# Performance work log

Hardware: AMD Instinct MI355X
Metric: run time of the kernel (lower is better)

The kernel has to match this reference:

```python
import jax, jax.numpy as jnp
import numpy as np

N, E, G = 50000, 1600000, 512
IN_DIM, HEADS, C1, C2, HIDDEN = 128, 3, 32, 32, 512
NEG_SLOPE = 0.2
EPS = 1e-16


def _glorot(key, shape):
    fan_in = shape[0]
    return jax.random.normal(key, shape, dtype=jnp.float32) / np.sqrt(fan_in)


def setup_inputs() -> dict:
    key = jax.random.key(0)
    ks = jax.random.split(key, 16)
    x = jax.random.normal(ks[0], (N, IN_DIM), dtype=jnp.float32)
    edge_index = jax.random.randint(ks[1], (2, E), 0, N, dtype=jnp.int64)
    batch = (jnp.arange(N, dtype=jnp.int64) * G) // N  # sorted, all graphs non-empty
    d1, d2 = HEADS * C1, HEADS * C2
    return {
        "x": x,
        "W_l1": _glorot(ks[2], (IN_DIM, d1)), "b_l1": jnp.zeros((d1,), jnp.float32),
        "W_r1": _glorot(ks[3], (IN_DIM, d1)), "b_r1": jnp.zeros((d1,), jnp.float32),
        "att1": _glorot(ks[4], (HEADS, C1)), "bias1": jnp.zeros((d1,), jnp.float32),
        "W_l2": _glorot(ks[5], (d1, d2)), "b_l2": jnp.zeros((d2,), jnp.float32),
        "W_r2": _glorot(ks[6], (d1, d2)), "b_r2": jnp.zeros((d2,), jnp.float32),
        "att2": _glorot(ks[7], (HEADS, C2)), "bias2": jnp.zeros((d2,), jnp.float32),
        "W_fc1": _glorot(ks[8], (d1 + d2, HIDDEN)), "b_fc1": jnp.zeros((HIDDEN,), jnp.float32),
        "W_fc2": _glorot(ks[9], (HIDDEN, 2)), "b_fc2": jnp.zeros((2,), jnp.float32),
        "edge_index": edge_index,
        "batch": batch,
    }


def gatv2_conv(xin, src, dst, W_l, b_l, W_r, b_r, att, bias, heads, out_c):
    n = xin.shape[0]
    x_l = (xin @ W_l + b_l).reshape(n, heads, out_c)  # source-side projection
    x_r = (xin @ W_r + b_r).reshape(n, heads, out_c)  # target-side projection
    e = jax.nn.leaky_relu(x_l[src] + x_r[dst], NEG_SLOPE)  # [E', H, C]
    logits = jnp.einsum("ehc,hc->eh", e, att)  # [E', H]
    m = jax.ops.segment_max(logits, dst, num_segments=n)
    a = jnp.exp(logits - m[dst])
    denom = jax.ops.segment_sum(a, dst, num_segments=n)
    alpha = a / (denom[dst] + EPS)  # per-destination edge softmax (PyG semantics)
    out = jax.ops.segment_sum(x_l[src] * alpha[:, :, None], dst, num_segments=n)
    return out.reshape(n, heads * out_c) + bias


def reference(x, W_l1, b_l1, W_r1, b_r1, att1, bias1,
              W_l2, b_l2, W_r2, b_r2, att2, bias2,
              W_fc1, b_fc1, W_fc2, b_fc2, edge_index, batch):
    n = x.shape[0]
    loop = jnp.arange(n, dtype=edge_index.dtype)
    src = jnp.concatenate([edge_index[0], loop])  # PyG GATv2Conv adds self-loops
    dst = jnp.concatenate([edge_index[1], loop])
    h1 = jnp.tanh(gatv2_conv(x, src, dst, W_l1, b_l1, W_r1, b_r1, att1, bias1, HEADS, C1))
    h2 = jnp.tanh(gatv2_conv(h1, src, dst, W_l2, b_l2, W_r2, b_r2, att2, bias2, HEADS, C2))
    h = jnp.concatenate([h1, h2], axis=1)  # [N, (C1+C2)*H]
    first_idx = jnp.searchsorted(batch, jnp.arange(G, dtype=batch.dtype))  # first node of each graph
    pooled = h[first_idx]  # [G, (C1+C2)*H]
    hidden = jax.nn.relu(pooled @ W_fc1 + b_fc1)
    logits = hidden @ W_fc2 + b_fc2
    return jax.nn.log_softmax(logits, axis=1)
```

## Files before the change

### kernel.cpp

```cpp
#include <hip/hip_runtime.h>
#include <hip/hip_bf16.h>
#include <hip/hip_fp16.h>
#include <math.h>

#define NN 50000
#define EE 1600000
#define GG 512
#define INDIM 128
#define HEADS 3
#define CC 32
#define DD 96
#define HID 512
#define NEG 0.2f
#define NEGM1 (NEG - 1.0f)
#define EPS_DEN 1e-16f
#define CAP 128
#define MNEG -1e30f
#define NBW 1568

#define OFF_WL1   0
#define OFF_BL1   12288
#define OFF_WR1   12384
#define OFF_BR1   24672
#define OFF_ATT1  24768
#define OFF_BIAS1 24864
#define OFF_WL2   24960
#define OFF_BL2   34176
#define OFF_WR2   34272
#define OFF_BR2   43488
#define OFF_ATT2  43584
#define OFF_BIAS2 43680
#define OFF_WFC1  43776
#define OFF_BFC1  142080
#define OFF_WFC2  142592
#define OFF_BFC2  143616
#define P_TOTAL   143744

typedef _Float16 h8 __attribute__((ext_vector_type(8)));
typedef float f4 __attribute__((ext_vector_type(4)));

static __device__ __forceinline__ float bf2f(__hip_bfloat16 v) { return __bfloat162float(v); }

static __device__ __forceinline__ int getI(const void* p, long long i, bool w64) {
    return w64 ? ((const int*)p)[2 * i] : ((const int*)p)[i];
}

static __device__ __forceinline__ void load4(const void* p, int base, int e0, bool w64, int* v) {
    const int4* q = (const int4*)p;
    if (w64) {
        int4 a = q[(base + e0) >> 1];
        int4 b = q[((base + e0) >> 1) + 1];
        v[0] = a.x; v[1] = a.z; v[2] = b.x; v[3] = b.z;
    } else {
        int4 a = q[(base + e0) >> 2];
        v[0] = a.x; v[1] = a.y; v[2] = a.z; v[3] = a.w;
    }
}

static __device__ __forceinline__ bool testbit(const unsigned* b, int i) {
    return (b[i >> 5] >> (i & 31)) & 1u;
}

__global__ void detect_kernel(const void* __restrict__ x, const void* __restrict__ ei,
                              int* __restrict__ flags)
{
    __shared__ int wild, zcnt;
    if (threadIdx.x == 0) { wild = 0; zcnt = 0; }
    __syncthreads();
    int w = 0, z = 0;
    const __hip_bfloat16* xb = (const __hip_bfloat16*)x;
    for (int i = threadIdx.x; i < 4096; i += 256) {
        float v = bf2f(xb[i]);
        if (!(fabsf(v) <= 1e6f)) w++;
    }
    const int* e32 = (const int*)ei;
    for (int i = threadIdx.x; i < 4096; i += 256) {
        if (e32[2 * i + 1] == 0) z++;
    }
    atomicAdd(&wild, w);
    atomicAdd(&zcnt, z);
    __syncthreads();
    if (threadIdx.x == 0) {
        flags[0] = (wild < 64) ? 1 : 0;
        flags[1] = (zcnt > 4000) ? 1 : 0;
    }
}

struct ParamTab { const void* p[16]; int sz[16]; int off[16]; };

__global__ void convert_params_kernel(ParamTab t, const int* __restrict__ flags,
                                      float* __restrict__ P)
{
    const int which = blockIdx.y;
    const int n = t.sz[which];
    const void* src = t.p[which];
    float* dst = P + t.off[which];
    const bool isbf = flags[0] != 0;
    for (int i = blockIdx.x * 256 + threadIdx.x; i < n; i += gridDim.x * 256) {
        dst[i] = isbf ? bf2f(((const __hip_bfloat16*)src)[i]) : ((const float*)src)[i];
    }
}

__global__ void build_bswz_kernel(const float* __restrict__ P, int offWl, int offWr, int KC,
                                  __half* __restrict__ B)
{
    int idx = blockIdx.x * 256 + threadIdx.x;
    int total = 12 * KC * 64;
    if (idx >= total) return;
    int lane = idx & 63;
    int t = idx >> 6;
    int kc = t % KC;
    int ntile = t / KC;
    int n = ntile * 16 + (lane & 15);
    int kbase = kc * 32 + (lane >> 4) * 8;
    const float* Wsrc = (n < 96) ? (P + offWl) : (P + offWr);
    int n2 = (n < 96) ? n : n - 96;
    __half* dst = B + (size_t)idx * 8;
#pragma unroll
    for (int j = 0; j < 8; j++) dst[j] = __float2half(Wsrc[(kbase + j) * 96 + n2]);
}

__global__ void build_bswz_fc_kernel(const float* __restrict__ P, __half* __restrict__ B)
{
    int idx = blockIdx.x * 256 + threadIdx.x;
    const int total = 32 * 6 * 64;
    if (idx >= total) return;
    int lane = idx & 63;
    int t = idx >> 6;
    int kc = t % 6;
    int ntile = t / 6;
    int n = ntile * 16 + (lane & 15);
    int kbase = kc * 32 + (lane >> 4) * 8;
    const float* W = P + OFF_WFC1;
    __half* dst = B + (size_t)idx * 8;
#pragma unroll
    for (int j = 0; j < 8; j++) dst[j] = __float2half(W[(kbase + j) * HID + n]);
}

__global__ void firstpool_kernel(const void* __restrict__ batch, const int* __restrict__ flags,
                                 int* __restrict__ first, unsigned* __restrict__ pb,
                                 unsigned* __restrict__ nb)
{
    int i = blockIdx.x * 256 + threadIdx.x;
    if (i >= NN) return;
    const bool w64 = flags[1] != 0;
    int b = getI(batch, i, w64);
    if (i == 0 || getI(batch, i - 1, w64) != b) {
        first[b] = i;
        atomicOr(&pb[i >> 5], 1u << (i & 31));
        atomicOr(&nb[i >> 5], 1u << (i & 31));
    }
}

__global__ void mark_needed_kernel(const void* __restrict__ ei, const int* __restrict__ flags,
                                   const unsigned* __restrict__ pb, unsigned* __restrict__ nb)
{
    int e0 = (blockIdx.x * 256 + threadIdx.x) * 4;
    if (e0 >= EE) return;
    const bool w64 = flags[1] != 0;
    int s4[4], d4[4];
    load4(ei, EE, e0, w64, d4);
    load4(ei, 0, e0, w64, s4);
#pragma unroll
    for (int j = 0; j < 4; j++)
        if (testbit(pb, d4[j])) atomicOr(&nb[s4[j] >> 5], 1u << (s4[j] & 31));
}

__global__ void compact_kernel(const unsigned* __restrict__ nb, int* __restrict__ list,
                               int* __restrict__ cnt)
{
    int i = blockIdx.x * 256 + threadIdx.x;
    if (i >= NN) return;
    if (testbit(nb, i)) list[atomicAdd(cnt, 1)] = i;
}

__global__ void scatter_fixed_kernel(const void* __restrict__ ei, const int* __restrict__ flags,
                                     const unsigned* __restrict__ nb,
                                     int* __restrict__ deg, int* __restrict__ csr)
{
    int e0 = (blockIdx.x * 256 + threadIdx.x) * 4;
    if (e0 >= EE) return;
    const bool w64 = flags[1] != 0;
    int s4[4], d4[4];
    load4(ei, EE, e0, w64, d4);
    load4(ei, 0, e0, w64, s4);
#pragma unroll
    for (int j = 0; j < 4; j++) {
        int dst = d4[j];
        if (!testbit(nb, dst)) continue;
        int pos = atomicAdd(&deg[dst], 1);
        if (pos < CAP) csr[(size_t)dst * CAP + pos] = s4[j];
    }
}

template <int KDIM, int MODE>
__global__ __launch_bounds__(256) void proj_mfma_kernel(
    const void* __restrict__ Ain, const __half* __restrict__ Bswz,
    const int* __restrict__ list, const int* __restrict__ cnt,
    const float* __restrict__ P, const int* __restrict__ flags, int offBl, int offBr,
    __half* __restrict__ xl, float* __restrict__ xr)
{
    constexpr int KC = KDIM / 32;
    __shared__ __half Bs[12 * KC * 64 * 8];
    const int tid = threadIdx.x;
    const int limit = MODE ? *cnt : NN;
    const int blockBase = blockIdx.x * 64;
    if (blockBase >= limit) return;

    {
        const int chunks = 12 * KC * 64;
        for (int i = tid; i < chunks; i += 256)
            reinterpret_cast<f4*>(Bs)[i] = reinterpret_cast<const f4*>(Bswz)[i];
    }
    __syncthreads();

    const int wave = tid >> 6;
    const int lane = tid & 63;
    const int base = blockBase + wave * 16;
    if (base >= limit) return;

    const int q = lane >> 4;
    const int mlane = lane & 15;

    int aIdx = base + mlane;
    int aRow;
    if (MODE) aRow = (aIdx < limit) ? list[aIdx] : list[limit - 1];
    else      aRow = (aIdx < limit) ? aIdx : 0;

    h8 a[KC];
    if (MODE == 1) {
        const h8* arow = reinterpret_cast<const h8*>((const __half*)Ain + (size_t)aRow * KDIM);
#pragma unroll
        for (int kc = 0; kc < KC; kc++) a[kc] = arow[kc * 4 + q];
    } else if (flags[0]) {
        const int4* arow = reinterpret_cast<const int4*>((const ushort*)Ain + (size_t)aRow * KDIM);
#pragma unroll
        for (int kc = 0; kc < KC; kc++) {
            int4 r = arow[kc * 4 + q];
            int ws[4] = {r.x, r.y, r.z, r.w};
#pragma unroll
            for (int i = 0; i < 4; i++) {
                a[kc][2 * i]     = (_Float16)__int_as_float(ws[i] << 16);
                a[kc][2 * i + 1] = (_Float16)__int_as_float(ws[i] & 0xffff0000);
            }
        }
    } else {
        const f4* arow = reinterpret_cast<const f4*>((const float*)Ain + (size_t)aRow * KDIM);
#pragma unroll
        for (int kc = 0; kc < KC; kc++) {
            f4 r0 = arow[kc * 8 + q * 2];
            f4 r1 = arow[kc * 8 + q * 2 + 1];
#pragma unroll
            for (int i = 0; i < 4; i++) {
                a[kc][i]     = (_Float16)r0[i];
                a[kc][4 + i] = (_Float16)r1[i];
            }
        }
    }

    int sRow[4];
#pragma unroll
    for (int r = 0; r < 4; r++) {
        int si = base + q * 4 + r;
        sRow[r] = (si < limit) ? (MODE ? list[si] : si) : -1;
    }

    const h8* Bf = reinterpret_cast<const h8*>(Bs);
#pragma unroll
    for (int ntile = 0; ntile < 12; ntile++) {
        int n = ntile * 16 + mlane;
        float bv = (n < 96) ? P[offBl + n] : P[offBr + n - 96];
        f4 acc = {bv, bv, bv, bv};
#pragma unroll
        for (int kc = 0; kc < KC; kc++) {
            h8 b = Bf[(ntile * KC + kc) * 64 + lane];
            acc = __builtin_amdgcn_mfma_f32_16x16x32_f16(a[kc], b, acc, 0, 0, 0);
        }
#pragma unroll
        for (int r = 0; r < 4; r++) {
            if (sRow[r] < 0) continue;
            if (n < 96) xl[(size_t)sRow[r] * DD + n] = __float2half(acc[r]);
            else        xr[(size_t)sRow[r] * DD + (n - 96)] = acc[r];
        }
    }
}

template <int OUTMODE>
__global__ __launch_bounds__(256) void fused_edge_kernel(
    const int* __restrict__ csr, const int* __restrict__ deg,
    const int* __restrict__ list, const int* __restrict__ cnt,
    const __half* __restrict__ xl, const float* __restrict__ xr,
    const float* __restrict__ P, int offAtt, int offBias,
    __half* __restrict__ out)
{
    const int lane = threadIdx.x & 63;
    const int c = lane & 31;
    const int eo = lane >> 5;
    const int w0 = (blockIdx.x * 256 + threadIdx.x) >> 6;
    const int nw = (gridDim.x * 256) >> 6;
    const int limit = (OUTMODE == 0) ? *cnt : GG;
    const int items = limit * 3;

    for (int item = w0; item < items; item += nw) {
        const int li = item / 3;
        const int h = item - li * 3;
        const int n = list[li];
        const int hc = h * CC + c;
        const __half* xlb = xl + hc;

        const float attc = P[offAtt + hc];
        const float xr_c = xr[(size_t)n * DD + hc];

        float m, d, o;
        {
            float xls = __half2float(xlb[n * DD]);
            float s = xls + xr_c;
            s = fmaf(fminf(s, 0.0f), NEGM1, s);
            float p = s * attc;
#pragma unroll
            for (int off = 16; off; off >>= 1) p += __shfl_xor(p, off, 32);
            if (eo == 0) { m = p; d = 1.0f; o = xls; }
            else         { m = MNEG; d = 0.0f; o = 0.0f; }
        }

        const int* row = csr + (size_t)n * CAP;
        const int end = min(deg[n], CAP);
        int k = eo;
        for (; k + 6 < end; k += 8) {
            int s0 = row[k], s1 = row[k + 2], s2 = row[k + 4], s3 = row[k + 6];
            float x0 = __half2float(xlb[s0 * DD]);
            float x1 = __half2float(xlb[s1 * DD]);
            float x2 = __half2float(xlb[s2 * DD]);
            float x3 = __half2float(xlb[s3 * DD]);
            float t0 = x0 + xr_c; t0 = fmaf(fminf(t0, 0.0f), NEGM1, t0);
            float t1 = x1 + xr_c; t1 = fmaf(fminf(t1, 0.0f), NEGM1, t1);
            float t2 = x2 + xr_c; t2 = fmaf(fminf(t2, 0.0f), NEGM1, t2);
            float t3 = x3 + xr_c; t3 = fmaf(fminf(t3, 0.0f), NEGM1, t3);
            float q0 = t0 * attc, q1 = t1 * attc, q2 = t2 * attc, q3 = t3 * attc;
#pragma unroll
            for (int off = 16; off; off >>= 1) {
                q0 += __shfl_xor(q0, off, 32);
                q1 += __shfl_xor(q1, off, 32);
                q2 += __shfl_xor(q2, off, 32);
                q3 += __shfl_xor(q3, off, 32);
            }
            if (q0 <= m) { float e = __expf(q0 - m); d += e; o += e * x0; }
            else         { float r2 = __expf(m - q0); d = d * r2 + 1.0f; o = o * r2 + x0; m = q0; }
            if (q1 <= m) { float e = __expf(q1 - m); d += e; o += e * x1; }
            else         { float r2 = __expf(m - q1); d = d * r2 + 1.0f; o = o * r2 + x1; m = q1; }
            if (q2 <= m) { float e = __expf(q2 - m); d += e; o += e * x2; }
            else         { float r2 = __expf(m - q2); d = d * r2 + 1.0f; o = o * r2 + x2; m = q2; }
            if (q3 <= m) { float e = __expf(q3 - m); d += e; o += e * x3; }
            else         { float r2 = __expf(m - q3); d = d * r2 + 1.0f; o = o * r2 + x3; m = q3; }
        }
        for (; k < end; k += 2) {
            int src = row[k];
            float xv = __half2float(xlb[src * DD]);
            float s = xv + xr_c;
            s = fmaf(fminf(s, 0.0f), NEGM1, s);
            float p = s * attc;
#pragma unroll
            for (int off = 16; off; off >>= 1) p += __shfl_xor(p, off, 32);
            if (p <= m) { float e = __expf(p - m); d += e; o += e * xv; }
            else        { float r2 = __expf(m - p); d = d * r2 + 1.0f; o = o * r2 + xv; m = p; }
        }

        float m2 = __shfl_xor(m, 32);
        float d2 = __shfl_xor(d, 32);
        float o2 = __shfl_xor(o, 32);
        float nm = fmaxf(m, m2);
        float e1 = __expf(m - nm), e2 = __expf(m2 - nm);
        d = d * e1 + d2 * e2;
        o = o * e1 + o2 * e2;

        float res = tanhf(o / (d + EPS_DEN) + P[offBias + hc]);
        if (eo == 0) {
            if (OUTMODE == 0) out[(size_t)n * DD + hc] = __float2half(res);
            else              out[(size_t)li * 192 + 96 + hc] = __float2half(res);
        }
    }
}

__global__ void gatherA_kernel(const __half* __restrict__ h1h, const int* __restrict__ first,
                               __half* __restrict__ A)
{
    int idx = blockIdx.x * 256 + threadIdx.x;
    if (idx >= GG * DD) return;
    int g = idx / DD, c = idx - g * DD;
    A[(size_t)g * 192 + c] = h1h[(size_t)first[g] * DD + c];
}

__global__ __launch_bounds__(256) void mlp_mfma_kernel(
    const __half* __restrict__ A, const __half* __restrict__ Bfc,
    const float* __restrict__ P, const int* __restrict__ flags, void* __restrict__ outv)
{
    const int tid = threadIdx.x;
    const int wave = tid >> 6, lane = tid & 63;
    const int q = lane >> 4, ml = lane & 15;
    const int rowbase = blockIdx.x * 64 + wave * 16;

    h8 a[6];
    const h8* arow = reinterpret_cast<const h8*>(A + (size_t)(rowbase + ml) * 192);
#pragma unroll
    for (int kc = 0; kc < 6; kc++) a[kc] = arow[kc * 4 + q];

    const h8* Bf = reinterpret_cast<const h8*>(Bfc);
    const float* w2 = P + OFF_WFC2;
    float p0[4] = {0, 0, 0, 0}, p1[4] = {0, 0, 0, 0};
    for (int nt = 0; nt < 32; nt++) {
        int n = nt * 16 + ml;
        float bv = P[OFF_BFC1 + n];
        f4 acc = {bv, bv, bv, bv};
#pragma unroll
        for (int kc = 0; kc < 6; kc++)
            acc = __builtin_amdgcn_mfma_f32_16x16x32_f16(a[kc], Bf[(nt * 6 + kc) * 64 + lane], acc, 0, 0, 0);
        float w20 = w2[2 * n], w21 = w2[2 * n + 1];
#pragma unroll
        for (int r = 0; r < 4; r++) {
            float hdn = fmaxf(acc[r], 0.0f);
            p0[r] = fmaf(hdn, w20, p0[r]);
            p1[r] = fmaf(hdn, w21, p1[r]);
        }
    }
#pragma unroll
    for (int off = 1; off <= 8; off <<= 1) {
#pragma unroll
        for (int r = 0; r < 4; r++) {
            p0[r] += __shfl_xor(p0[r], off);
            p1[r] += __shfl_xor(p1[r], off);
        }
    }
    if (ml == 0) {
        float b0 = P[OFF_BFC2], b1 = P[OFF_BFC2 + 1];
#pragma unroll
        for (int r = 0; r < 4; r++) {
            int g = rowbase + q * 4 + r;
            float l0 = p0[r] + b0, l1 = p1[r] + b1;
            float mx = fmaxf(l0, l1);
            float lse = mx + logf(__expf(l0 - mx) + __expf(l1 - mx));
            if (flags[0]) {
                ((__hip_bfloat16*)outv)[g * 2 + 0] = __float2bfloat16(l0 - lse);
                ((__hip_bfloat16*)outv)[g * 2 + 1] = __float2bfloat16(l1 - lse);
            } else {
                ((float*)outv)[g * 2 + 0] = l0 - lse;
                ((float*)outv)[g * 2 + 1] = l1 - lse;
            }
        }
    }
}

extern "C" void kernel_launch(void* const* d_in, const int* in_sizes, int n_in,
                              void* d_out, int out_size, void* d_ws, size_t ws_size,
                              hipStream_t stream)
{
    const void* x     = d_in[0];
    const void* ei    = d_in[17];
    const void* batch = d_in[18];

    float* ws   = (float*)d_ws;
    float* P    = ws;
    float* xr   = P + P_TOTAL;

    __half* hp   = (__half*)(xr + (size_t)NN * DD);
    __half* xlh  = hp;
    __half* xl2h = xlh + (size_t)NN * DD;
    __half* h1h  = xl2h + (size_t)NN * DD;
    __half* A    = h1h + (size_t)NN * DD;
    __half* B1   = A + (size_t)GG * 192;
    __half* B2   = B1 + 24576;
    __half* Bfc  = B2 + 18432;

    int* ip       = (int*)(Bfc + 98304);
    int* deg      = ip;
    unsigned* pb  = (unsigned*)(deg + NN);
    unsigned* nb  = pb + NBW;
    int* cnt      = (int*)(nb + NBW);
    int* csr      = cnt + 4;
    int* list     = csr + (size_t)NN * CAP;
    int* first    = list + NN;
    int* flags    = first + GG;

    ParamTab t;
    const int sz[16]  = {12288, 96, 12288, 96, 96, 96, 9216, 96, 9216, 96, 96, 96, 98304, 512, 1024, 2};
    const int off[16] = {OFF_WL1, OFF_BL1, OFF_WR1, OFF_BR1, OFF_ATT1, OFF_BIAS1,
                         OFF_WL2, OFF_BL2, OFF_WR2, OFF_BR2, OFF_ATT2, OFF_BIAS2,
                         OFF_WFC1, OFF_BFC1, OFF_WFC2, OFF_BFC2};
    for (int i = 0; i < 16; i++) { t.p[i] = d_in[1 + i]; t.sz[i] = sz[i]; t.off[i] = off[i]; }

    const int edge4B = (EE / 4 + 255) / 256;
    const int nodeB = (NN + 255) / 256;
    const int mprojB = (NN + 63) / 64;
    const int fuse1B = 2048;
    const int fuse2B = (GG * 3) / 4;

    detect_kernel<<<1, 256, 0, stream>>>(x, ei, flags);
    convert_params_kernel<<<dim3(96, 16), 256, 0, stream>>>(t, flags, P);
    build_bswz_kernel<<<12, 256, 0, stream>>>(P, OFF_WL1, OFF_WR1, 4, B1);
    build_bswz_kernel<<<9, 256, 0, stream>>>(P, OFF_WL2, OFF_WR2, 3, B2);
    build_bswz_fc_kernel<<<48, 256, 0, stream>>>(P, Bfc);
    (void)hipMemsetAsync(deg, 0, (size_t)(NN + 2 * NBW + 4) * sizeof(int), stream);

    firstpool_kernel<<<nodeB, 256, 0, stream>>>(batch, flags, first, pb, nb);
    mark_needed_kernel<<<edge4B, 256, 0, stream>>>(ei, flags, pb, nb);
    compact_kernel<<<nodeB, 256, 0, stream>>>(nb, list, cnt);

    scatter_fixed_kernel<<<edge4B, 256, 0, stream>>>(ei, flags, nb, deg, csr);

    proj_mfma_kernel<INDIM, 0><<<mprojB, 256, 0, stream>>>(x, B1, nullptr, nullptr,
                                                           P, flags, OFF_BL1, OFF_BR1, xlh, xr);
    fused_edge_kernel<0><<<fuse1B, 256, 0, stream>>>(csr, deg, list, cnt, xlh, xr,
                                                     P, OFF_ATT1, OFF_BIAS1, h1h);

    proj_mfma_kernel<DD, 1><<<mprojB, 256, 0, stream>>>(h1h, B2, list, cnt,
                                                        P, flags, OFF_BL2, OFF_BR2, xl2h, xr);
    fused_edge_kernel<1><<<fuse2B, 256, 0, stream>>>(csr, deg, first, nullptr, xl2h, xr,
                                                     P, OFF_ATT2, OFF_BIAS2, A);

    gatherA_kernel<<<(GG * DD + 255) / 256, 256, 0, stream>>>(h1h, first, A);
    mlp_mfma_kernel<<<GG / 64, 256, 0, stream>>>(A, Bfc, P, flags, d_out);
}
```

Before: 297.5 us.

## Merge setup and preprocessing kernels to cut launch count

Several small setup kernels (parameter conversion, three B-swizzle builds, memset, first-node pooling) are collapsed into one multi-task setup kernel that reads raw inputs directly, so the full weights are no longer staged as fp32. The needed-node bitmask, built with atomicOr, becomes an int array written with plain stores. The compaction step now runs as an extra grid dimension of the scatter kernel. The gatherA kernel is removed: the MLP kernel reads the h1 rows via first[] and the layer-2 output from a smaller A2 buffer. The aim is to cut launch overhead and serialization, at the cost of a larger needed array and branchy multi-task kernels.

```diff
diff --git a/kernel.cpp b/kernel.cpp
--- a/kernel.cpp
+++ b/kernel.cpp
@@ -18,23 +18,18 @@
 #define MNEG -1e30f
 #define NBW 1568
 
-#define OFF_WL1   0
-#define OFF_BL1   12288
-#define OFF_WR1   12384
-#define OFF_BR1   24672
-#define OFF_ATT1  24768
-#define OFF_BIAS1 24864
-#define OFF_WL2   24960
-#define OFF_BL2   34176
-#define OFF_WR2   34272
-#define OFF_BR2   43488
-#define OFF_ATT2  43584
-#define OFF_BIAS2 43680
-#define OFF_WFC1  43776
-#define OFF_BFC1  142080
-#define OFF_WFC2  142592
-#define OFF_BFC2  143616
-#define P_TOTAL   143744
+#define PS_BL1   0
+#define PS_BR1   96
+#define PS_ATT1  192
+#define PS_BIAS1 288
+#define PS_BL2   384
+#define PS_BR2   480
+#define PS_ATT2  576
+#define PS_BIAS2 672
+#define PS_BFC1  768
+#define PS_WFC2  1280
+#define PS_BFC2  2304
+#define PS_TOTAL 2308
 
 typedef _Float16 h8 __attribute__((ext_vector_type(8)));
 typedef float f4 __attribute__((ext_vector_type(4)));
@@ -43,6 +38,10 @@
 
 static __device__ __forceinline__ int getI(const void* p, long long i, bool w64) {
     return w64 ? ((const int*)p)[2 * i] : ((const int*)p)[i];
+}
+
+static __device__ __forceinline__ float rawf(const void* p, int i, bool isbf) {
+    return isbf ? bf2f(((const __hip_bfloat16*)p)[i]) : ((const float*)p)[i];
 }
 
 static __device__ __forceinline__ void load4(const void* p, int base, int e0, bool w64, int* v) {
@@ -86,74 +85,88 @@
     }
 }
 
-struct ParamTab { const void* p[16]; int sz[16]; int off[16]; };
-
-__global__ void convert_params_kernel(ParamTab t, const int* __restrict__ flags,
-                                      float* __restrict__ P)
-{
-    const int which = blockIdx.y;
-    const int n = t.sz[which];
-    const void* src = t.p[which];
-    float* dst = P + t.off[which];
+struct SetupArgs {
+    const void *wl1, *wr1, *wl2, *wr2, *wfc1;
+    const void *bl1, *br1, *att1, *bias1, *bl2, *br2, *att2, *bias2, *bfc1, *wfc2, *bfc2;
+    const void *batch;
+};
+
+__global__ void setup_kernel(SetupArgs a, const int* __restrict__ flags,
+                             float* __restrict__ P, __half* __restrict__ B1,
+                             __half* __restrict__ B2, __half* __restrict__ Bfc,
+                             int* __restrict__ deg, int* __restrict__ needed,
+                             int* __restrict__ first, unsigned* __restrict__ pb,
+                             int* __restrict__ cnt)
+{
+    const int task = blockIdx.y;
+    const int idx = blockIdx.x * 256 + threadIdx.x;
     const bool isbf = flags[0] != 0;
-    for (int i = blockIdx.x * 256 + threadIdx.x; i < n; i += gridDim.x * 256) {
-        dst[i] = isbf ? bf2f(((const __hip_bfloat16*)src)[i]) : ((const float*)src)[i];
-    }
-}
-
-__global__ void build_bswz_kernel(const float* __restrict__ P, int offWl, int offWr, int KC,
-                                  __half* __restrict__ B)
-{
-    int idx = blockIdx.x * 256 + threadIdx.x;
-    int total = 12 * KC * 64;
-    if (idx >= total) return;
-    int lane = idx & 63;
-    int t = idx >> 6;
-    int kc = t % KC;
-    int ntile = t / KC;
-    int n = ntile * 16 + (lane & 15);
-    int kbase = kc * 32 + (lane >> 4) * 8;
-    const float* Wsrc = (n < 96) ? (P + offWl) : (P + offWr);
-    int n2 = (n < 96) ? n : n - 96;
-    __half* dst = B + (size_t)idx * 8;
-#pragma unroll
-    for (int j = 0; j < 8; j++) dst[j] = __float2half(Wsrc[(kbase + j) * 96 + n2]);
-}
-
-__global__ void build_bswz_fc_kernel(const float* __restrict__ P, __half* __restrict__ B)
-{
-    int idx = blockIdx.x * 256 + threadIdx.x;
-    const int total = 32 * 6 * 64;
-    if (idx >= total) return;
-    int lane = idx & 63;
-    int t = idx >> 6;
-    int kc = t % 6;
-    int ntile = t / 6;
-    int n = ntile * 16 + (lane & 15);
-    int kbase = kc * 32 + (lane >> 4) * 8;
-    const float* W = P + OFF_WFC1;
-    __half* dst = B + (size_t)idx * 8;
-#pragma unroll
-    for (int j = 0; j < 8; j++) dst[j] = __float2half(W[(kbase + j) * HID + n]);
-}
-
-__global__ void firstpool_kernel(const void* __restrict__ batch, const int* __restrict__ flags,
-                                 int* __restrict__ first, unsigned* __restrict__ pb,
-                                 unsigned* __restrict__ nb)
-{
-    int i = blockIdx.x * 256 + threadIdx.x;
-    if (i >= NN) return;
-    const bool w64 = flags[1] != 0;
-    int b = getI(batch, i, w64);
-    if (i == 0 || getI(batch, i - 1, w64) != b) {
-        first[b] = i;
-        atomicOr(&pb[i >> 5], 1u << (i & 31));
-        atomicOr(&nb[i >> 5], 1u << (i & 31));
+
+    if (task == 0) {
+        if (idx == 0) *cnt = 0;
+        if (idx >= PS_TOTAL) return;
+        const void* src; int rel;
+        if (idx < 768) {
+            int k = idx / 96; rel = idx - k * 96;
+            const void* s8[8] = {a.bl1, a.br1, a.att1, a.bias1, a.bl2, a.br2, a.att2, a.bias2};
+            src = s8[k];
+        } else if (idx < 1280) { src = a.bfc1; rel = idx - 768; }
+        else if (idx < 2304)   { src = a.wfc2; rel = idx - 1280; }
+        else if (idx < 2306)   { src = a.bfc2; rel = idx - 2304; }
+        else return;
+        P[idx] = rawf(src, rel, isbf);
+    } else if (task == 1 || task == 2) {
+        const int KC = (task == 1) ? 4 : 3;
+        const int total = 12 * KC * 64;
+        if (idx >= total) return;
+        int lane = idx & 63, t = idx >> 6;
+        int kc = t % KC, ntile = t / KC;
+        int n = ntile * 16 + (lane & 15);
+        int kbase = kc * 32 + (lane >> 4) * 8;
+        const void* W = (task == 1) ? (n < 96 ? a.wl1 : a.wr1) : (n < 96 ? a.wl2 : a.wr2);
+        int n2 = (n < 96) ? n : n - 96;
+        __half* dst = ((task == 1) ? B1 : B2) + (size_t)idx * 8;
+#pragma unroll
+        for (int j = 0; j < 8; j++) dst[j] = __float2half(rawf(W, (kbase + j) * 96 + n2, isbf));
+    } else if (task == 3) {
+        const int total = 32 * 6 * 64;
+        if (idx >= total) return;
+        int lane = idx & 63, t = idx >> 6;
+        int kc = t % 6, ntile = t / 6;
+        int n = ntile * 16 + (lane & 15);
+        int kbase = kc * 32 + (lane >> 4) * 8;
+        __half* dst = Bfc + (size_t)idx * 8;
+#pragma unroll
+        for (int j = 0; j < 8; j++) dst[j] = __float2half(rawf(a.wfc1, (kbase + j) * HID + n, isbf));
+    } else if (task == 4) {
+        int i0 = idx * 4;
+#pragma unroll
+        for (int j = 0; j < 4; j++) if (i0 + j < NN) deg[i0 + j] = 0;
+    } else if (task == 5) {
+        if (idx >= NN) return;
+        const bool w64 = flags[1] != 0;
+        int b = getI(a.batch, idx, w64);
+        bool isf = (idx == 0) || (getI(a.batch, idx - 1, w64) != b);
+        needed[idx] = isf ? 1 : 0;
+        if (isf) first[b] = idx;
+    } else {
+        if (idx >= NBW) return;
+        const bool w64 = flags[1] != 0;
+        unsigned word = 0;
+        int prev = (idx == 0) ? -1 : getI(a.batch, idx * 32 - 1, w64);
+        for (int bit = 0; bit < 32; bit++) {
+            int i = idx * 32 + bit;
+            if (i >= NN) break;
+            int b = getI(a.batch, i, w64);
+            if (i == 0 || b != prev) word |= (1u << bit);
+            prev = b;
+        }
+        pb[idx] = word;
     }
 }
 
 __global__ void mark_needed_kernel(const void* __restrict__ ei, const int* __restrict__ flags,
-                                   const unsigned* __restrict__ pb, unsigned* __restrict__ nb)
+                                   const unsigned* __restrict__ pb, int* __restrict__ needed)
 {
     int e0 = (blockIdx.x * 256 + threadIdx.x) * 4;
     if (e0 >= EE) return;
@@ -163,21 +176,20 @@
     load4(ei, 0, e0, w64, s4);
 #pragma unroll
     for (int j = 0; j < 4; j++)
-        if (testbit(pb, d4[j])) atomicOr(&nb[s4[j] >> 5], 1u << (s4[j] & 31));
-}
-
-__global__ void compact_kernel(const unsigned* __restrict__ nb, int* __restrict__ list,
-                               int* __restrict__ cnt)
-{
-    int i = blockIdx.x * 256 + threadIdx.x;
-    if (i >= NN) return;
-    if (testbit(nb, i)) list[atomicAdd(cnt, 1)] = i;
-}
-
-__global__ void scatter_fixed_kernel(const void* __restrict__ ei, const int* __restrict__ flags,
-                                     const unsigned* __restrict__ nb,
-                                     int* __restrict__ deg, int* __restrict__ csr)
-{
+        if (testbit(pb, d4[j])) needed[s4[j]] = 1;
+}
+
+__global__ void scatter_compact_kernel(const void* __restrict__ ei, const int* __restrict__ flags,
+                                       const int* __restrict__ needed,
+                                       int* __restrict__ deg, int* __restrict__ csr,
+                                       int* __restrict__ list, int* __restrict__ cnt)
+{
+    if (blockIdx.y == 1) {
+        int i = blockIdx.x * 256 + threadIdx.x;
+        if (i >= NN) return;
+        if (needed[i]) list[atomicAdd(cnt, 1)] = i;
+        return;
+    }
     int e0 = (blockIdx.x * 256 + threadIdx.x) * 4;
     if (e0 >= EE) return;
     const bool w64 = flags[1] != 0;
@@ -187,7 +199,7 @@
 #pragma unroll
     for (int j = 0; j < 4; j++) {
         int dst = d4[j];
-        if (!testbit(nb, dst)) continue;
+        if (!needed[dst]) continue;
         int pos = atomicAdd(&deg[dst], 1);
         if (pos < CAP) csr[(size_t)dst * CAP + pos] = s4[j];
     }
@@ -376,40 +388,38 @@
         float res = tanhf(o / (d + EPS_DEN) + P[offBias + hc]);
         if (eo == 0) {
             if (OUTMODE == 0) out[(size_t)n * DD + hc] = __float2half(res);
-            else              out[(size_t)li * 192 + 96 + hc] = __float2half(res);
-        }
-    }
-}
-
-__global__ void gatherA_kernel(const __half* __restrict__ h1h, const int* __restrict__ first,
-                               __half* __restrict__ A)
-{
-    int idx = blockIdx.x * 256 + threadIdx.x;
-    if (idx >= GG * DD) return;
-    int g = idx / DD, c = idx - g * DD;
-    A[(size_t)g * 192 + c] = h1h[(size_t)first[g] * DD + c];
+            else              out[(size_t)li * DD + hc] = __float2half(res);
+        }
+    }
 }
 
 __global__ __launch_bounds__(256) void mlp_mfma_kernel(
-    const __half* __restrict__ A, const __half* __restrict__ Bfc,
+    const __half* __restrict__ h1h, const __half* __restrict__ A2,
+    const int* __restrict__ first, const __half* __restrict__ Bfc,
     const float* __restrict__ P, const int* __restrict__ flags, void* __restrict__ outv)
 {
     const int tid = threadIdx.x;
     const int wave = tid >> 6, lane = tid & 63;
     const int q = lane >> 4, ml = lane & 15;
     const int rowbase = blockIdx.x * 64 + wave * 16;
+    const int g16 = rowbase + ml;
 
     h8 a[6];
-    const h8* arow = reinterpret_cast<const h8*>(A + (size_t)(rowbase + ml) * 192);
-#pragma unroll
-    for (int kc = 0; kc < 6; kc++) a[kc] = arow[kc * 4 + q];
+    {
+        const h8* l = reinterpret_cast<const h8*>(h1h + (size_t)first[g16] * DD);
+#pragma unroll
+        for (int kc = 0; kc < 3; kc++) a[kc] = l[kc * 4 + q];
+        const h8* r = reinterpret_cast<const h8*>(A2 + (size_t)g16 * DD);
+#pragma unroll
+        for (int kc = 3; kc < 6; kc++) a[kc] = r[(kc - 3) * 4 + q];
+    }
 
     const h8* Bf = reinterpret_cast<const h8*>(Bfc);
-    const float* w2 = P + OFF_WFC2;
+    const float* w2 = P + PS_WFC2;
     float p0[4] = {0, 0, 0, 0}, p1[4] = {0, 0, 0, 0};
     for (int nt = 0; nt < 32; nt++) {
         int n = nt * 16 + ml;
-        float bv = P[OFF_BFC1 + n];
+        float bv = P[PS_BFC1 + n];
         f4 acc = {bv, bv, bv, bv};
 #pragma unroll
         for (int kc = 0; kc < 6; kc++)
@@ -431,7 +441,7 @@
         }
     }
     if (ml == 0) {
-        float b0 = P[OFF_BFC2], b1 = P[OFF_BFC2 + 1];
+        float b0 = P[PS_BFC2], b1 = P[PS_BFC2 + 1];
 #pragma unroll
         for (int r = 0; r < 4; r++) {
             int g = rowbase + q * 4 + r;
@@ -459,63 +469,56 @@
 
     float* ws   = (float*)d_ws;
     float* P    = ws;
-    float* xr   = P + P_TOTAL;
+    float* xr   = P + PS_TOTAL;
 
     __half* hp   = (__half*)(xr + (size_t)NN * DD);
     __half* xlh  = hp;
     __half* xl2h = xlh + (size_t)NN * DD;
     __half* h1h  = xl2h + (size_t)NN * DD;
-    __half* A    = h1h + (size_t)NN * DD;
-    __half* B1   = A + (size_t)GG * 192;
+    __half* A2   = h1h + (size_t)NN * DD;
+    __half* B1   = A2 + (size_t)GG * DD;
     __half* B2   = B1 + 24576;
     __half* Bfc  = B2 + 18432;
 
     int* ip       = (int*)(Bfc + 98304);
     int* deg      = ip;
-    unsigned* pb  = (unsigned*)(deg + NN);
-    unsigned* nb  = pb + NBW;
-    int* cnt      = (int*)(nb + NBW);
+    int* needed   = deg + NN;
+    int* cnt      = needed + NN;
     int* csr      = cnt + 4;
     int* list     = csr + (size_t)NN * CAP;
     int* first    = list + NN;
     int* flags    = first + GG;
-
-    ParamTab t;
-    const int sz[16]  = {12288, 96, 12288, 96, 96, 96, 9216, 96, 9216, 96, 96, 96, 98304, 512, 1024, 2};
-    const int off[16] = {OFF_WL1, OFF_BL1, OFF_WR1, OFF_BR1, OFF_ATT1, OFF_BIAS1,
-                         OFF_WL2, OFF_BL2, OFF_WR2, OFF_BR2, OFF_ATT2, OFF_BIAS2,
-                         OFF_WFC1, OFF_BFC1, OFF_WFC2, OFF_BFC2};
-    for (int i = 0; i < 16; i++) { t.p[i] = d_in[1 + i]; t.sz[i] = sz[i]; t.off[i] = off[i]; }
+    unsigned* pb  = (unsigned*)(flags + 4);
+
+    SetupArgs sa;
+    sa.wl1 = d_in[1];  sa.bl1 = d_in[2];  sa.wr1 = d_in[3];  sa.br1 = d_in[4];
+    sa.att1 = d_in[5]; sa.bias1 = d_in[6];
+    sa.wl2 = d_in[7];  sa.bl2 = d_in[8];  sa.wr2 = d_in[9];  sa.br2 = d_in[10];
+    sa.att2 = d_in[11]; sa.bias2 = d_in[12];
+    sa.wfc1 = d_in[13]; sa.bfc1 = d_in[14]; sa.wfc2 = d_in[15]; sa.bfc2 = d_in[16];
+    sa.batch = batch;
 
     const int edge4B = (EE / 4 + 255) / 256;
-    const int nodeB = (NN + 255) / 256;
     const int mprojB = (NN + 63) / 64;
     const int fuse1B = 2048;
     const int fuse2B = (GG * 3) / 4;
 
     detect_kernel<<<1, 256, 0, stream>>>(x, ei, flags);
-    convert_params_kernel<<<dim3(96, 16), 256, 0, stream>>>(t, flags, P);
-    build_bswz_kernel<<<12, 256, 0, stream>>>(P, OFF_WL1, OFF_WR1, 4, B1);
-    build_bswz_kernel<<<9, 256, 0, stream>>>(P, OFF_WL2, OFF_WR2, 3, B2);
-    build_bswz_fc_kernel<<<48, 256, 0, stream>>>(P, Bfc);
-    (void)hipMemsetAsync(deg, 0, (size_t)(NN + 2 * NBW + 4) * sizeof(int), stream);
-
-    firstpool_kernel<<<nodeB, 256, 0, stream>>>(batch, flags, first, pb, nb);
-    mark_needed_kernel<<<edge4B, 256, 0, stream>>>(ei, flags, pb, nb);
-    compact_kernel<<<nodeB, 256, 0, stream>>>(nb, list, cnt);
-
-    scatter_fixed_kernel<<<edge4B, 256, 0, stream>>>(ei, flags, nb, deg, csr);
+    setup_kernel<<<dim3(196, 7), 256, 0, stream>>>(sa, flags, P, B1, B2, Bfc,
+                                                   deg, needed, first, pb, cnt);
+    mark_needed_kernel<<<edge4B, 256, 0, stream>>>(ei, flags, pb, needed);
+    scatter_compact_kernel<<<dim3(edge4B, 2), 256, 0, stream>>>(ei, flags, needed,
+                                                                deg, csr, list, cnt);
 
     proj_mfma_kernel<INDIM, 0><<<mprojB, 256, 0, stream>>>(x, B1, nullptr, nullptr,
-                                                           P, flags, OFF_BL1, OFF_BR1, xlh, xr);
+                                                           P, flags, PS_BL1, PS_BR1, xlh, xr);
     fused_edge_kernel<0><<<fuse1B, 256, 0, stream>>>(csr, deg, list, cnt, xlh, xr,
-                                                     P, OFF_ATT1, OFF_BIAS1, h1h);
+                                                     P, PS_ATT1, PS_BIAS1, h1h);
 
     proj_mfma_kernel<DD, 1><<<mprojB, 256, 0, stream>>>(h1h, B2, list, cnt,
-                                                        P, flags, OFF_BL2, OFF_BR2, xl2h, xr);
+                                                        P, flags, PS_BL2, PS_BR2, xl2h, xr);
     fused_edge_kernel<1><<<fuse2B, 256, 0, stream>>>(csr, deg, first, nullptr, xl2h, xr,
-                                                     P, OFF_ATT2, OFF_BIAS2, A);
-
-    gatherA_kernel<<<(GG * DD + 255) / 256, 256, 0, stream>>>(h1h, first, A);
-    mlp_mfma_kernel<<<GG / 64, 256, 0, stream>>>(A, Bfc, P, flags, d_out);
-}
+                                                     P, PS_ATT2, PS_BIAS2, A2);
+
+    mlp_mfma_kernel<<<GG / 64, 256, 0, stream>>>(h1h, A2, first, Bfc, P, flags, d_out);
+}
```

Result: faster. 284.7 us (-4.3%).
